# Performance work log

Measured on AMD Instinct MI355X. Metric: run time of the kernel, lower is better.

## Reference

```python
import jax, jax.numpy as jnp
import numpy as np

WINDOW = 128  # window_length (overlap-and-add hop); K = 2*WINDOW


def setup_inputs() -> dict:
    key = jax.random.key(0)
    k_x, k_w1, k_b1, k_w2, k_b2 = jax.random.split(key, 5)
    B, D, K, S = 4, 128, 256, 256      # batch, in_channels, segment len, n segments
    C, E, O = 2, 128, 256              # source_num, encoded_frame_dim, out_channels
    x = jax.random.normal(k_x, (B, D, K, S), dtype=jnp.float32)
    prelu_w = jnp.asarray(0.25, dtype=jnp.float32)  # nn.PReLU default init
    conv1_w = jax.random.normal(k_w1, (C * E, D), dtype=jnp.float32) * 0.02
    conv1_b = jax.random.normal(k_b1, (C * E,), dtype=jnp.float32) * 0.02
    conv2_w = jax.random.normal(k_w2, (O, E), dtype=jnp.float32) * 0.02
    conv2_b = jax.random.normal(k_b2, (O,), dtype=jnp.float32) * 0.02
    return {
        "x": x,
        "prelu_w": prelu_w,
        "conv1_w": conv1_w,
        "conv1_b": conv1_b,
        "conv2_w": conv2_w,
        "conv2_b": conv2_b,
        "pad_front": 64,
        "pad_back": 64,
    }


def overlap_and_add(y, hop):
    # y: [B, C, E, S, K] -> [B, C, E, hop*(S-1)+K] windowed scatter-sum
    B, C, E, S, K = y.shape
    T = hop * (S - 1) + K
    idx = (hop * jnp.arange(S)[:, None] + jnp.arange(K)[None, :]).reshape(-1)  # [S*K]
    out = jnp.zeros((B, C, E, T), dtype=y.dtype)
    return out.at[..., idx].add(y.reshape(B, C, E, S * K))


def reference(x, prelu_w, conv1_w, conv1_b, conv2_w, conv2_b, pad_front, pad_back):
    B, D, K, S = x.shape
    E = conv2_w.shape[1]
    C = conv1_w.shape[0] // E
    # PReLU (single shared parameter)
    x = jnp.where(x >= 0, x, prelu_w * x)
    # 1x1 Conv2d: D -> C*E channels (pure GEMM over channel dim)
    x = jnp.einsum('bdks,od->boks', x, conv1_w) + conv1_b[None, :, None, None]
    # split sources/features, move K to last: [B, C, E, S, K]
    x = x.reshape(B, C, E, K, S).transpose(0, 1, 2, 4, 3)
    x = overlap_and_add(x, WINDOW)  # [B, C, E, T]
    T = x.shape[-1]
    end = T - pad_back if pad_back else T  # replicate [pad_front:-pad_back] slicing
    x = x[:, :, :, pad_front:end]          # [B, C, E, L]
    x = jax.nn.relu(x)
    # 1x1 Conv1d: E -> O
    x = jnp.einsum('bcel,oe->bcol', x, conv2_w) + conv2_b[None, None, :, None]
    return x  # [B, C, O, L]
```

## Files before the change

### kernel.cpp

```cpp
#include <hip/hip_runtime.h>
#include <hip/hip_bf16.h>
#include <stdint.h>

#define B_   4
#define D_   128
#define K_   256
#define S_   256
#define O_   256
#define E_   128
#define LOUT 32768

typedef __attribute__((ext_vector_type(8))) short short8;
typedef __attribute__((ext_vector_type(4))) float float4v;

__device__ __forceinline__ unsigned short f2bf(float f) {
  union { float f; unsigned u; } v; v.f = f;
  unsigned r = v.u + 0x7FFF + ((v.u >> 16) & 1);
  return (unsigned short)(r >> 16);
}

__device__ __forceinline__ void gl_lds16(const void* g, void* l) {
  __builtin_amdgcn_global_load_lds(
      (const __attribute__((address_space(1))) void*)g,
      (__attribute__((address_space(3))) void*)l, 16, 0, 0);
}

__global__ void pack_w_kernel(const float* __restrict__ w1, const float* __restrict__ w2,
                              unsigned short* __restrict__ w1p, unsigned short* __restrict__ w2p) {
  int i = blockIdx.x * 256 + threadIdx.x;
  w1p[i] = f2bf(w1[i]);
  w2p[i] = f2bf(w2[i]);
}

__global__ __launch_bounds__(256) void pack_x_kernel(const float* __restrict__ x,
                                                     const float* __restrict__ prelu_w,
                                                     unsigned short* __restrict__ xp) {
  __shared__ float tile[64][65];
  int k  = blockIdx.x;
  int st = blockIdx.y & 3;
  int dt = blockIdx.y >> 2;
  int b  = blockIdx.z;
  float pw = *prelu_w;
  int t = threadIdx.x;

  {
    int s4  = (t & 15) * 4;
    int dl0 = t >> 4;
    const float* src = x + ((size_t)(b * D_ + dt * 64) * K_ + k) * S_ + st * 64 + s4;
#pragma unroll
    for (int i = 0; i < 4; ++i) {
      int dl = dl0 + i * 16;
      float4v v = *(const float4v*)(src + (size_t)dl * (K_ * S_));
#pragma unroll
      for (int r = 0; r < 4; ++r) {
        float f = v[r];
        tile[dl][s4 + r] = (f >= 0.f) ? f : f * pw;
      }
    }
  }
  __syncthreads();
  {
    int d8 = (t & 7) * 8;
    int sx = t >> 3;
#pragma unroll
    for (int i = 0; i < 2; ++i) {
      int sl = sx + i * 32;
      short8 o;
#pragma unroll
      for (int e = 0; e < 8; ++e) o[e] = (short)f2bf(tile[d8 + e][sl]);
      int s = st * 64 + sl;
      *(short8*)(xp + (((size_t)(b * S_ + s) * K_ + k) * D_ + dt * 64 + d8)) = o;
    }
  }
}

__global__ __launch_bounds__(256, 2) void fused_kernel(
    const unsigned short* __restrict__ xp,
    const unsigned short* __restrict__ w1p,
    const unsigned short* __restrict__ w2p,
    const float* __restrict__ b1,
    const float* __restrict__ b2,
    float* __restrict__ out) {
  __shared__ __align__(16) unsigned char lds[65536];

  int j = blockIdx.x;
  int b = blockIdx.y;
  int t = threadIdx.x;
  int w  = t >> 6;
  int ln64 = t & 63;
  int q  = ln64 >> 4;
  int ln = ln64 & 15;

  bool va = (j < S_);
  bool vb = (j >= 1);

  {
    bool myv = (w < 2) ? va : vb;
    if (myv) {
      int s = (w < 2) ? j : (j - 1);
      for (int i = 0; i < 16; ++i) {
        int row = (w * 16 + i) * 4 + q;
        int dblk = ln ^ (row & 15);
        const unsigned short* g = xp + (((size_t)(b * S_ + s) * K_ + row) * D_ + dblk * 8);
        gl_lds16((const void*)g, (void*)(lds + (w * 16 + i) * 1024));
      }
    }
  }

  int mtg = w * 4;
  short8 a1[4][4];
  float4v b1v[4];
  for (int m = 0; m < 4; ++m) {
    int o = (mtg + m) * 16 + ln;
    for (int ks = 0; ks < 4; ++ks)
      a1[m][ks] = *(const short8*)(w1p + (size_t)o * D_ + ks * 32 + q * 8);
    b1v[m] = *(const float4v*)(b1 + (mtg + m) * 16 + q * 4);
  }
  float bmul = (va ? 1.f : 0.f) + (vb ? 1.f : 0.f);

  __syncthreads();

  int c = w >> 1;
  int ebase = (w & 1) * 64;

  for (int p = 0; p < 8; ++p) {
    float4v acca[4], accb[4];
    for (int m = 0; m < 4; ++m) { acca[m] = (float4v)0.f; accb[m] = (float4v)0.f; }
    if (va) {
      int row = p * 16 + ln;
      for (int ks = 0; ks < 4; ++ks) {
        short8 bf = *(const short8*)(lds + row * 256 + (((ks * 4 + q) ^ ln) * 16));
        for (int m = 0; m < 4; ++m)
          acca[m] = __builtin_amdgcn_mfma_f32_16x16x32_bf16(a1[m][ks], bf, acca[m], 0, 0, 0);
      }
    }
    if (vb) {
      int row = 128 + p * 16 + ln;
      for (int ks = 0; ks < 4; ++ks) {
        short8 bf = *(const short8*)(lds + row * 256 + (((ks * 4 + q) ^ ln) * 16));
        for (int m = 0; m < 4; ++m)
          accb[m] = __builtin_amdgcn_mfma_f32_16x16x32_bf16(a1[m][ks], bf, accb[m], 0, 0, 0);
      }
    }
    __syncthreads();
    int k1 = p * 16 + ln;
    for (int m = 0; m < 4; ++m) {
      float4v zf = acca[m] + accb[m] + b1v[m] * bmul;
      unsigned long long pk =
          (unsigned long long)f2bf(fmaxf(zf[0], 0.f))
        | ((unsigned long long)f2bf(fmaxf(zf[1], 0.f)) << 16)
        | ((unsigned long long)f2bf(fmaxf(zf[2], 0.f)) << 32)
        | ((unsigned long long)f2bf(fmaxf(zf[3], 0.f)) << 48);
      int e0 = ebase + m * 16 + q * 4;
      *(unsigned long long*)(lds + (c * 128 + k1) * 256 + ((e0 >> 3) ^ ln) * 16 + (e0 & 7) * 2) = pk;
    }
  }

  short8 w2f[4][4];
  float  b2s[4];
  for (int n = 0; n < 4; ++n) {
    int o2 = w * 64 + n * 16 + ln;
    for (int ks = 0; ks < 4; ++ks)
      w2f[n][ks] = *(const short8*)(w2p + (size_t)o2 * E_ + ks * 32 + q * 8);
    b2s[n] = b2[o2];
  }

  __syncthreads();

  for (int cc = 0; cc < 2; ++cc) {
    for (int m = 0; m < 8; ++m) {
      short8 zf[4];
#pragma unroll
      for (int ks = 0; ks < 4; ++ks)
        zf[ks] = *(const short8*)(lds + (cc * 128 + m * 16 + ln) * 256 + (((ks * 4 + q) ^ ln) * 16));
      float4v acc[4];
#pragma unroll
      for (int n = 0; n < 4; ++n) acc[n] = (float4v)0.f;
#pragma unroll
      for (int ks = 0; ks < 4; ++ks)
#pragma unroll
        for (int n = 0; n < 4; ++n)
          acc[n] = __builtin_amdgcn_mfma_f32_16x16x32_bf16(zf[ks], w2f[n][ks], acc[n], 0, 0, 0);
      int lpos = j * 128 + m * 16 + q * 4 - 64;
      if (lpos >= 0 && lpos < LOUT) {
#pragma unroll
        for (int n = 0; n < 4; ++n) {
          float4v sv;
#pragma unroll
          for (int r = 0; r < 4; ++r) sv[r] = acc[n][r] + b2s[n];
          *(float4v*)(out + ((size_t)(b * 2 + cc) * 256 + w * 64 + n * 16 + ln) * LOUT + lpos) = sv;
        }
      }
    }
  }
}

extern "C" void kernel_launch(void* const* d_in, const int* in_sizes, int n_in,
                              void* d_out, int out_size, void* d_ws, size_t ws_size,
                              hipStream_t stream) {
  const float* x       = (const float*)d_in[0];
  const float* prelu_w = (const float*)d_in[1];
  const float* w1      = (const float*)d_in[2];
  const float* b1      = (const float*)d_in[3];
  const float* w2      = (const float*)d_in[4];
  const float* b2      = (const float*)d_in[5];

  unsigned short* xp  = (unsigned short*)d_ws;
  unsigned short* w1p = xp + (size_t)B_ * S_ * K_ * D_;
  unsigned short* w2p = w1p + (size_t)O_ * D_;

  pack_w_kernel<<<dim3(128), 256, 0, stream>>>(w1, w2, w1p, w2p);
  pack_x_kernel<<<dim3(K_, 8, B_), 256, 0, stream>>>(x, prelu_w, xp);
  fused_kernel<<<dim3(S_ + 1, B_), 256, 0, stream>>>(xp, w1p, w2p, b1, b2,
                                                     (float*)d_out);
}
```

Before: 426.7 us.

## Fold weight packing into x-pack kernel, widen pack tiles, and batch GEMM1 steps

Removes the separate weight-packing launch by having batch-0 blocks of the x-pack kernel convert conv weights to bf16. The x-pack kernel now processes all 128 input channels per block (a 128x65 tile), writing full 256-byte channel rows and halving the grid. In the fused kernel, the first GEMM loop handles two 16-row K-slices per iteration, which halves the number of barriers and gives more independent MFMA chains, at the cost of more accumulator registers.

```diff
diff --git a/kernel.cpp b/kernel.cpp
--- a/kernel.cpp
+++ b/kernel.cpp
@@ -25,30 +25,31 @@
       (__attribute__((address_space(3))) void*)l, 16, 0, 0);
 }
 
-__global__ void pack_w_kernel(const float* __restrict__ w1, const float* __restrict__ w2,
-                              unsigned short* __restrict__ w1p, unsigned short* __restrict__ w2p) {
-  int i = blockIdx.x * 256 + threadIdx.x;
-  w1p[i] = f2bf(w1[i]);
-  w2p[i] = f2bf(w2[i]);
-}
-
 __global__ __launch_bounds__(256) void pack_x_kernel(const float* __restrict__ x,
                                                      const float* __restrict__ prelu_w,
-                                                     unsigned short* __restrict__ xp) {
-  __shared__ float tile[64][65];
+                                                     unsigned short* __restrict__ xp,
+                                                     const float* __restrict__ w1,
+                                                     const float* __restrict__ w2,
+                                                     unsigned short* __restrict__ w1p,
+                                                     unsigned short* __restrict__ w2p) {
+  __shared__ float tile[128][65];
   int k  = blockIdx.x;
-  int st = blockIdx.y & 3;
-  int dt = blockIdx.y >> 2;
+  int st = blockIdx.y;
   int b  = blockIdx.z;
   float pw = *prelu_w;
   int t = threadIdx.x;
 
+  if (b == 0) {
+    int lid = (st * 256 + k) * 256 + t;
+    if (lid < 32768) { w1p[lid] = f2bf(w1[lid]); w2p[lid] = f2bf(w2[lid]); }
+  }
+
   {
     int s4  = (t & 15) * 4;
     int dl0 = t >> 4;
-    const float* src = x + ((size_t)(b * D_ + dt * 64) * K_ + k) * S_ + st * 64 + s4;
-#pragma unroll
-    for (int i = 0; i < 4; ++i) {
+    const float* src = x + ((size_t)b * D_ * K_ + k) * S_ + st * 64 + s4;
+#pragma unroll
+    for (int i = 0; i < 8; ++i) {
       int dl = dl0 + i * 16;
       float4v v = *(const float4v*)(src + (size_t)dl * (K_ * S_));
 #pragma unroll
@@ -60,16 +61,16 @@
   }
   __syncthreads();
   {
-    int d8 = (t & 7) * 8;
-    int sx = t >> 3;
-#pragma unroll
-    for (int i = 0; i < 2; ++i) {
-      int sl = sx + i * 32;
+    int d8  = (t & 15) * 8;
+    int sl0 = t >> 4;
+#pragma unroll
+    for (int i = 0; i < 4; ++i) {
+      int sl = sl0 + i * 16;
       short8 o;
 #pragma unroll
       for (int e = 0; e < 8; ++e) o[e] = (short)f2bf(tile[d8 + e][sl]);
       int s = st * 64 + sl;
-      *(short8*)(xp + (((size_t)(b * S_ + s) * K_ + k) * D_ + dt * 64 + d8)) = o;
+      *(short8*)(xp + (((size_t)(b * S_ + s) * K_ + k) * D_ + d8)) = o;
     }
   }
 }
@@ -123,36 +124,43 @@
   int c = w >> 1;
   int ebase = (w & 1) * 64;
 
-  for (int p = 0; p < 8; ++p) {
-    float4v acca[4], accb[4];
-    for (int m = 0; m < 4; ++m) { acca[m] = (float4v)0.f; accb[m] = (float4v)0.f; }
+  for (int p2 = 0; p2 < 4; ++p2) {
+    float4v acca[2][4], accb[2][4];
+    for (int h = 0; h < 2; ++h)
+      for (int m = 0; m < 4; ++m) { acca[h][m] = (float4v)0.f; accb[h][m] = (float4v)0.f; }
     if (va) {
-      int row = p * 16 + ln;
-      for (int ks = 0; ks < 4; ++ks) {
-        short8 bf = *(const short8*)(lds + row * 256 + (((ks * 4 + q) ^ ln) * 16));
-        for (int m = 0; m < 4; ++m)
-          acca[m] = __builtin_amdgcn_mfma_f32_16x16x32_bf16(a1[m][ks], bf, acca[m], 0, 0, 0);
+      for (int h = 0; h < 2; ++h) {
+        int row = p2 * 32 + h * 16 + ln;
+        for (int ks = 0; ks < 4; ++ks) {
+          short8 bf = *(const short8*)(lds + row * 256 + (((ks * 4 + q) ^ ln) * 16));
+          for (int m = 0; m < 4; ++m)
+            acca[h][m] = __builtin_amdgcn_mfma_f32_16x16x32_bf16(a1[m][ks], bf, acca[h][m], 0, 0, 0);
+        }
       }
     }
     if (vb) {
-      int row = 128 + p * 16 + ln;
-      for (int ks = 0; ks < 4; ++ks) {
-        short8 bf = *(const short8*)(lds + row * 256 + (((ks * 4 + q) ^ ln) * 16));
-        for (int m = 0; m < 4; ++m)
-          accb[m] = __builtin_amdgcn_mfma_f32_16x16x32_bf16(a1[m][ks], bf, accb[m], 0, 0, 0);
+      for (int h = 0; h < 2; ++h) {
+        int row = 128 + p2 * 32 + h * 16 + ln;
+        for (int ks = 0; ks < 4; ++ks) {
+          short8 bf = *(const short8*)(lds + row * 256 + (((ks * 4 + q) ^ ln) * 16));
+          for (int m = 0; m < 4; ++m)
+            accb[h][m] = __builtin_amdgcn_mfma_f32_16x16x32_bf16(a1[m][ks], bf, accb[h][m], 0, 0, 0);
+        }
       }
     }
     __syncthreads();
-    int k1 = p * 16 + ln;
-    for (int m = 0; m < 4; ++m) {
-      float4v zf = acca[m] + accb[m] + b1v[m] * bmul;
-      unsigned long long pk =
-          (unsigned long long)f2bf(fmaxf(zf[0], 0.f))
-        | ((unsigned long long)f2bf(fmaxf(zf[1], 0.f)) << 16)
-        | ((unsigned long long)f2bf(fmaxf(zf[2], 0.f)) << 32)
-        | ((unsigned long long)f2bf(fmaxf(zf[3], 0.f)) << 48);
-      int e0 = ebase + m * 16 + q * 4;
-      *(unsigned long long*)(lds + (c * 128 + k1) * 256 + ((e0 >> 3) ^ ln) * 16 + (e0 & 7) * 2) = pk;
+    for (int h = 0; h < 2; ++h) {
+      int k1 = p2 * 32 + h * 16 + ln;
+      for (int m = 0; m < 4; ++m) {
+        float4v zf = acca[h][m] + accb[h][m] + b1v[m] * bmul;
+        unsigned long long pk =
+            (unsigned long long)f2bf(fmaxf(zf[0], 0.f))
+          | ((unsigned long long)f2bf(fmaxf(zf[1], 0.f)) << 16)
+          | ((unsigned long long)f2bf(fmaxf(zf[2], 0.f)) << 32)
+          | ((unsigned long long)f2bf(fmaxf(zf[3], 0.f)) << 48);
+        int e0 = ebase + m * 16 + q * 4;
+        *(unsigned long long*)(lds + (c * 128 + k1) * 256 + ((e0 >> 3) ^ ln) * 16 + (e0 & 7) * 2) = pk;
+      }
     }
   }
 
@@ -209,8 +217,7 @@
   unsigned short* w1p = xp + (size_t)B_ * S_ * K_ * D_;
   unsigned short* w2p = w1p + (size_t)O_ * D_;
 
-  pack_w_kernel<<<dim3(128), 256, 0, stream>>>(w1, w2, w1p, w2p);
-  pack_x_kernel<<<dim3(K_, 8, B_), 256, 0, stream>>>(x, prelu_w, xp);
+  pack_x_kernel<<<dim3(K_, 4, B_), 256, 0, stream>>>(x, prelu_w, xp, w1, w2, w1p, w2p);
   fused_kernel<<<dim3(S_ + 1, B_), 256, 0, stream>>>(xp, w1p, w2p, b1, b2,
                                                      (float*)d_out);
 }
```

New measurement: 426.7 us. About the same (+0.0%).
